# Optimization experiments

Measured on AMD Instinct MI355X. Metric: run time of the kernel, lower is better.

The kernel has to match this reference:

```python
import jax, jax.numpy as jnp
import numpy as np
from jax import lax

NC = 10        # tess_size
EPS = 1e-07


def cpab_basis(nc):
    # Constraint matrix L @ Avees = 0, Avees = [a0,b0,a1,b1,...] per cell.
    # Continuity at interior knots x_i = i/nc, plus zero-boundary v(0)=v(1)=0.
    L = np.zeros((nc + 1, 2 * nc))
    for i in range(1, nc):
        xi = i / nc
        L[i - 1, 2 * (i - 1):2 * i] = [xi, 1.0]
        L[i - 1, 2 * i:2 * i + 2] = [-xi, -1.0]
    L[nc - 1, 1] = 1.0                      # v(0) = b_0 = 0
    L[nc, 2 * nc - 2:2 * nc] = [1.0, 1.0]   # v(1) = a_{nc-1} + b_{nc-1} = 0
    U, S, Vh = np.linalg.svd(L)
    rank = int((S > 1e-8 * S[0]).sum())
    return np.ascontiguousarray(Vh[rank:].T).astype(np.float32)  # (2*nc, nc-1)


def mlp(x1, W0, b0, W1, b1, W2, b2, W3, b3):
    h = jax.nn.relu(x1 @ W0 + b0)
    h = jax.nn.relu(h @ W1 + b1)
    h = jax.nn.relu(h @ W2 + b2)
    return h @ W3 + b3


def integrate_cpab(x, A, nc):
    # x: [N] in (0,1); A: [N, nc, 2] per-cell (slope a, intercept b).
    # Closed-form integration of dphi/dt = a_c*phi + b_c for t in [0,1],
    # walking across cells. Also accumulates s = integral of a(phi(t)) dt,
    # so dphi/dx = exp(s)  (space gradient of the transform).
    a_all = A[..., 0]
    b_all = A[..., 1]
    fnc = jnp.asarray(nc, x.dtype)
    c0 = jnp.clip(jnp.floor(x * nc).astype(jnp.int32), 0, nc - 1)

    def step(carry, _):
        phi, c, t, s, done = carry
        a = jnp.take_along_axis(a_all, c[:, None], 1)[:, 0]
        b = jnp.take_along_axis(b_all, c[:, None], 1)[:, 0]
        v = a * phi + b
        big = jnp.abs(a) > 1e-10
        a_safe = jnp.where(big, a, 1.0)
        # closed-form solution with remaining time t
        psi = jnp.where(big, (phi + b / a_safe) * jnp.exp(a * t) - b / a_safe,
                        phi + b * t)
        lo = c.astype(x.dtype) / fnc
        hi = (c + 1).astype(x.dtype) / fnc
        inside = (psi >= lo) & (psi <= hi)
        xc = jnp.where(v >= 0, hi, lo)          # boundary hit in flow direction
        vb = a * xc + b
        v_safe = jnp.where(v == 0, 1.0, v)
        ratio = jnp.maximum(vb / v_safe, 1e-30)
        t_hit = jnp.where(big, jnp.log(ratio) / a_safe, (xc - phi) / v_safe)
        act = ~done
        cross = act & ~inside
        s = s + jnp.where(act, a * jnp.where(inside, t, t_hit), 0.0)
        phi = jnp.where(cross, xc, jnp.where(act & inside, psi, phi))
        t = jnp.where(cross, t - t_hit, t)
        c = jnp.clip(jnp.where(cross, c + jnp.where(v >= 0, 1, -1), c), 0, nc - 1)
        done = done | inside
        return (phi, c, t, s, done), None

    init = (x, c0, jnp.ones_like(x), jnp.zeros_like(x),
            jnp.zeros(x.shape, bool))
    (phi, _, _, s, _), _ = lax.scan(step, init, None, length=nc + 1)
    return phi, jnp.exp(s)


def _forward(x, B, W0, b0, W1, b1, W2, b2, W3, b3):
    mask = jnp.array([1, 0])  # left=True
    x = jnp.clip(x, EPS, 1.0 - EPS)
    xm = x[:, mask]
    x1, x2 = xm[:, :1], xm[:, 1:]          # [N,1] each
    theta = mlp(x1, W0, b0, W1, b1, W2, b2, W3, b3)   # [N, nc-1]
    A = (theta @ B.T).reshape(-1, NC, 2)    # per-cell (a, b)
    z2, dz2 = integrate_cpab(x2[:, 0], A, NC)
    z = jnp.column_stack([x1[:, 0], z2])[:, mask]
    log_dz_dx = jnp.column_stack([jnp.zeros_like(x1[:, 0]),
                                  jnp.log(dz2)])[:, mask]
    return z, log_dz_dx


def setup_inputs() -> dict:
    key = jax.random.key(0)
    ks = jax.random.split(key, 9)
    N, H, D = 4_194_304, 10, NC - 1
    x = jax.random.uniform(ks[0], (N, 2), jnp.float32)
    sc = 0.5
    return {
        'x': x,
        'B': jnp.asarray(cpab_basis(NC)),
        'W0': jax.random.normal(ks[1], (1, H), jnp.float32) * sc,
        'b0': jax.random.normal(ks[2], (H,), jnp.float32) * 0.1,
        'W1': jax.random.normal(ks[3], (H, H), jnp.float32) * sc,
        'b1': jax.random.normal(ks[4], (H,), jnp.float32) * 0.1,
        'W2': jax.random.normal(ks[5], (H, H), jnp.float32) * sc,
        'b2': jax.random.normal(ks[6], (H,), jnp.float32) * 0.1,
        'W3': jax.random.normal(ks[7], (H, D), jnp.float32) * sc,
        'b3': jax.random.normal(ks[8], (D,), jnp.float32) * 0.1,
    }


def reference(x, B, W0, b0, W1, b1, W2, b2, W3, b3):
    return _forward(x, B, W0, b0, W1, b1, W2, b2, W3, b3)
```

## Files before the change

kernel.cpp:

```cpp
#include <hip/hip_runtime.h>
#include <math.h>

#define NCELL 10
#define TPTS  512
#define BLK   1024

__device__ __forceinline__ float satf(float v) {
    return fminf(fmaxf(v, -3.389e38f), 3.389e38f);
}

__global__ __launch_bounds__(256) void table_kernel(
    const float* __restrict__ B,
    const float* __restrict__ W0, const float* __restrict__ b0,
    const float* __restrict__ W1, const float* __restrict__ b1,
    const float* __restrict__ W2, const float* __restrict__ b2,
    const float* __restrict__ W3, const float* __restrict__ b3,
    float* __restrict__ tab, float lo, float hi, float dx)
{
    const int i = blockIdx.x * 256 + threadIdx.x;
    if (i >= TPTS) return;
    float x1 = fmaf((float)i, dx, lo);
    if (i == TPTS - 1) x1 = hi;

    float h0[10], h1[10], h2[10];
    #pragma unroll
    for (int j = 0; j < 10; ++j)
        h0[j] = fmaxf(fmaf(x1, W0[j], b0[j]), 0.0f);
    #pragma unroll
    for (int j = 0; j < 10; ++j) {
        float acc = b1[j];
        #pragma unroll
        for (int k = 0; k < 10; ++k) acc = fmaf(h0[k], W1[k * 10 + j], acc);
        h1[j] = fmaxf(acc, 0.0f);
    }
    #pragma unroll
    for (int j = 0; j < 10; ++j) {
        float acc = b2[j];
        #pragma unroll
        for (int k = 0; k < 10; ++k) acc = fmaf(h1[k], W2[k * 10 + j], acc);
        h2[j] = fmaxf(acc, 0.0f);
    }
    float theta[9];
    #pragma unroll
    for (int j = 0; j < 9; ++j) {
        float acc = b3[j];
        #pragma unroll
        for (int k = 0; k < 10; ++k) acc = fmaf(h2[k], W3[k * 9 + j], acc);
        theta[j] = acc;
    }
    #pragma unroll
    for (int j = 1; j <= 9; ++j) {
        float aj = 0.f, bj = 0.f;
        #pragma unroll
        for (int q = 0; q < 9; ++q) {
            aj = fmaf(theta[q], B[(2 * j) * 9 + q], aj);
            bj = fmaf(theta[q], B[(2 * j + 1) * 9 + q], bj);
        }
        tab[(j - 1) * TPTS + i] = fmaf(aj, (float)j / 10.0f, bj);
    }
}

__global__ __launch_bounds__(BLK) void cpab_kernel(
    const float* __restrict__ x,
    const float* __restrict__ tab,
    float* __restrict__ out, int N,
    float lo, float inv_dx)
{
    __shared__ float sT[9 * TPTS];

    const int tid = threadIdx.x;

    {
        const float4* g4 = reinterpret_cast<const float4*>(tab);
        float4* s4 = reinterpret_cast<float4*>(sT);
        #pragma unroll
        for (int k = tid; k < 9 * TPTS / 4; k += BLK) s4[k] = g4[k];
    }
    __syncthreads();

    const int i = blockIdx.x * BLK + tid;
    if (i >= N) return;

    const float2 xv = reinterpret_cast<const float2*>(x)[i];
    const float hi_clip = 1.0f - 1e-7f;
    const float x2 = fminf(fmaxf(xv.x, 1e-7f), hi_clip);
    const float x1 = fminf(fmaxf(xv.y, 1e-7f), hi_clip);

    const float tt  = (x1 - lo) * inv_dx;
    const int  cell = min((int)tt, TPTS - 2);
    const float f   = tt - (float)cell;

    const float* base = sT + cell;
    auto node = [&](int j) -> float {
        const int jj = (min(max(j, 1), 9) - 1) * TPTS;
        const float v0 = base[jj];
        const float v1 = base[jj + 1];
        const float v  = fmaf(f, v1 - v0, v0);
        return (j >= 1 && j <= 9) ? v : 0.0f;
    };

    const float p10  = x2 * 10.0f;
    const int   cc0  = (int)p10;
    const float frac = p10 - (float)cc0;
    const float nc = node(cc0);
    const float nn = node(cc0 + 1);
    const float a0s = (nn - nc) * 10.0f;
    const float u0 = fmaf(nn - nc, frac, nc);
    const bool  right = (u0 >= 0.0f);
    const float d10   = right ? 10.0f : -10.0f;
    const int   dint  = right ? 1 : -1;

    float p  = x2;
    float u  = u0;
    float ru = __builtin_amdgcn_rcpf(u0);
    int   cn = cc0 + (right ? 1 : 0);
    float w  = right ? nn : nc;
    float t  = 1.0f;
    float a  = 0.0f, ra = 1.0f;
    bool  big = false;

    #pragma unroll 1
    for (int it = 0; ; ++it) {
        a   = (w - u) * d10;
        big = fabsf(a) > 1e-10f;
        ra  = __builtin_amdgcn_rcpf(big ? a : 1.0f);
        const float q  = w * ru;
        const float lg = __logf(q);
        const float xc = (float)cn * 0.1f;
        const float t_hit = big ? (lg * ra) : ((xc - p) * ru);
        if (!(t_hit < t) || it >= 11) break;
        t  -= t_hit;
        p   = xc;
        u   = w;
        ru  = __builtin_amdgcn_rcpf(w);
        cn += dint;
        w   = node(cn);
    }

    const float e   = __expf(a * t);
    float phi = big ? fmaf(u * ra, e - 1.0f, p) : fmaf(u, t, p);
    const float ru0 = __builtin_amdgcn_rcpf(u0);
    float ldz = __logf(fabsf(u * e * ru0));
    if (u0 == 0.0f) { phi = x2; ldz = a0s; }

    reinterpret_cast<float2*>(out)[i] = make_float2(satf(phi), x1);
    reinterpret_cast<float2*>(out + (size_t)2 * N)[i] = make_float2(satf(ldz), 0.0f);
}

extern "C" void kernel_launch(void* const* d_in, const int* in_sizes, int n_in,
                              void* d_out, int out_size, void* d_ws, size_t ws_size,
                              hipStream_t stream) {
    (void)n_in; (void)out_size; (void)ws_size;
    const float* x  = (const float*)d_in[0];
    const float* B  = (const float*)d_in[1];
    const float* W0 = (const float*)d_in[2];
    const float* b0 = (const float*)d_in[3];
    const float* W1 = (const float*)d_in[4];
    const float* b1 = (const float*)d_in[5];
    const float* W2 = (const float*)d_in[6];
    const float* b2 = (const float*)d_in[7];
    const float* W3 = (const float*)d_in[8];
    const float* b3 = (const float*)d_in[9];
    float* ws  = (float*)d_ws;
    float* out = (float*)d_out;

    const int N = in_sizes[0] / 2;
    const float lo = 1e-7f, hi = 1.0f - 1e-7f;
    const float dx = (hi - lo) / (float)(TPTS - 1);
    const float inv_dx = (float)(TPTS - 1) / (hi - lo);

    table_kernel<<<(TPTS + 255) / 256, 256, 0, stream>>>(
        B, W0, b0, W1, b1, W2, b2, W3, b3, ws, lo, hi, dx);
    cpab_kernel<<<(N + BLK - 1) / BLK, BLK, 0, stream>>>(
        x, ws, out, N, lo, inv_dx);
}
```

Measured before the change: 121.8 us.

## Replace divergent cell-walk loop with fully unrolled branchless prefix-sum over cells

Swaps the data-dependent cell-crossing loop for a fixed, fully unrolled pass. It precomputes the node velocities and their logs for all ten possible cells ahead, sums the hit times, and picks the final cell state by selects. The aim is to remove warp divergence and the serial node-lookup, log and rcp chain per iteration. In exchange every thread always does ten LDS loads and eleven logs. The log-derivative is now computed additively in log space, which can round differently.

New measurement: 142.4 us. 1.17x slower.

```diff
diff --git a/kernel.cpp b/kernel.cpp
--- a/kernel.cpp
+++ b/kernel.cpp
@@ -69,7 +69,6 @@
     __shared__ float sT[9 * TPTS];
 
     const int tid = threadIdx.x;
-
     {
         const float4* g4 = reinterpret_cast<const float4*>(tab);
         float4* s4 = reinterpret_cast<float4*>(sT);
@@ -82,14 +81,13 @@
     if (i >= N) return;
 
     const float2 xv = reinterpret_cast<const float2*>(x)[i];
-    const float hi_clip = 1.0f - 1e-7f;
-    const float x2 = fminf(fmaxf(xv.x, 1e-7f), hi_clip);
-    const float x1 = fminf(fmaxf(xv.y, 1e-7f), hi_clip);
+    const float hic = 1.0f - 1e-7f;
+    const float x2 = fminf(fmaxf(xv.x, 1e-7f), hic);
+    const float x1 = fminf(fmaxf(xv.y, 1e-7f), hic);
 
     const float tt  = (x1 - lo) * inv_dx;
     const int  cell = min((int)tt, TPTS - 2);
     const float f   = tt - (float)cell;
-
     const float* base = sT + cell;
     auto node = [&](int j) -> float {
         const int jj = (min(max(j, 1), 9) - 1) * TPTS;
@@ -100,48 +98,66 @@
     };
 
     const float p10  = x2 * 10.0f;
-    const int   cc0  = (int)p10;
+    const int   cc0  = min((int)p10, 9);
     const float frac = p10 - (float)cc0;
     const float nc = node(cc0);
     const float nn = node(cc0 + 1);
-    const float a0s = (nn - nc) * 10.0f;
+    const float a0 = (nn - nc) * 10.0f;
     const float u0 = fmaf(nn - nc, frac, nc);
     const bool  right = (u0 >= 0.0f);
     const float d10   = right ? 10.0f : -10.0f;
     const int   dint  = right ? 1 : -1;
+    const int   s0    = cc0 + (right ? 1 : 0);
 
-    float p  = x2;
-    float u  = u0;
-    float ru = __builtin_amdgcn_rcpf(u0);
-    int   cn = cc0 + (right ? 1 : 0);
-    float w  = right ? nn : nc;
-    float t  = 1.0f;
-    float a  = 0.0f, ra = 1.0f;
-    bool  big = false;
+    float m[10], l[10];
+    m[0] = right ? nn : nc;
+    #pragma unroll
+    for (int k = 1; k < 10; ++k) {
+        const int sk = min(max(s0 + k * dint, 0), 10);
+        m[k] = node(sk);
+    }
+    const float lu0 = __logf(fabsf(u0));
+    #pragma unroll
+    for (int k = 0; k < 10; ++k) l[k] = __logf(fabsf(m[k]));
 
-    #pragma unroll 1
-    for (int it = 0; ; ++it) {
-        a   = (w - u) * d10;
-        big = fabsf(a) > 1e-10f;
-        ra  = __builtin_amdgcn_rcpf(big ? a : 1.0f);
-        const float q  = w * ru;
-        const float lg = __logf(q);
-        const float xc = (float)cn * 0.1f;
-        const float t_hit = big ? (lg * ra) : ((xc - p) * ru);
-        if (!(t_hit < t) || it >= 11) break;
-        t  -= t_hit;
-        p   = xc;
-        u   = w;
-        ru  = __builtin_amdgcn_rcpf(w);
-        cn += dint;
-        w   = node(cn);
+    float T = 0.0f;
+    float Tc = 0.0f;
+    int   K = 0;
+    float u_st = u0, l_st = lu0, a_st = 0.0f, ra_st = 1.0f;
+    bool  prevCrossed = false;
+
+    #pragma unroll
+    for (int k = 0; k < 10; ++k) {
+        const float pm = (k == 0) ? u0  : m[k - 1];
+        const float pl = (k == 0) ? lu0 : l[k - 1];
+        const float a  = (k == 0) ? a0  : (m[k] - m[k - 1]) * d10;
+        const float as = copysignf(fmaxf(fabsf(a), 1e-10f), a);
+        const float ra = __builtin_amdgcn_rcpf(as);
+        const bool  ss  = (m[k] * pm) > 0.0f;
+        const float tau = ss ? ((l[k] - pl) * ra) : 1e30f;
+        T += tau;
+        const bool crossed = (T < 1.0f);
+        if (k == 0) { a_st = as; ra_st = ra; }
+        else {
+            a_st  = prevCrossed ? as : a_st;
+            ra_st = prevCrossed ? ra : ra_st;
+        }
+        u_st = crossed ? m[k] : u_st;
+        l_st = crossed ? l[k] : l_st;
+        Tc   = crossed ? T    : Tc;
+        K   += crossed ? 1    : 0;
+        prevCrossed = crossed;
     }
 
-    const float e   = __expf(a * t);
-    float phi = big ? fmaf(u * ra, e - 1.0f, p) : fmaf(u, t, p);
-    const float ru0 = __builtin_amdgcn_rcpf(u0);
-    float ldz = __logf(fabsf(u * e * ru0));
-    if (u0 == 0.0f) { phi = x2; ldz = a0s; }
+    const float t_rem = 1.0f - Tc;
+    const float p_st  = (K == 0) ? x2
+                      : (float)(s0 + (K - 1) * dint) * 0.1f;
+    const bool  big   = fabsf(a_st) > 1e-10f;
+    const float e     = __expf(a_st * t_rem);
+    float phi = big ? fmaf(u_st * ra_st, e - 1.0f, p_st)
+                    : fmaf(u_st, t_rem, p_st);
+    float ldz = fmaf(a_st, t_rem, l_st - lu0);
+    if (u0 == 0.0f) { phi = x2; ldz = a0; }
 
     reinterpret_cast<float2*>(out)[i] = make_float2(satf(phi), x1);
     reinterpret_cast<float2*>(out + (size_t)2 * N)[i] = make_float2(satf(ldz), 0.0f);
```
